# Kernel tuning notes

Hardware: AMD Instinct MI355X
Metric: run time of the kernel (lower is better)

Reference implementation:

```python
import jax, jax.numpy as jnp
import numpy as np

# ---- box encoding helpers ----

def _cv2_corners(b):
    # b: [..., 5] (cx, cy, w, h, angle) -> [..., 4, 2] rotated-rect vertices
    cx, cy, w, h, a = (b[..., i] for i in range(5))
    c, s = jnp.cos(a), jnp.sin(a)
    dx, dy = w * 0.5, h * 0.5
    lx = jnp.stack([-dx, dx, dx, -dx], axis=-1)   # [..., 4]
    ly = jnp.stack([-dy, -dy, dy, dy], axis=-1)
    x = cx[..., None] + lx * c[..., None] - ly * s[..., None]
    y = cy[..., None] + lx * s[..., None] + ly * c[..., None]
    return jnp.stack([x, y], axis=-1)


def _vertices_to_cv2(v):
    # v: [..., 4, 2] ordered vertices -> [..., 5] (cx, cy, w, h, angle)
    ctr = v.mean(axis=-2)
    e1 = v[..., 1, :] - v[..., 0, :]
    e2 = v[..., 3, :] - v[..., 0, :]
    w = jnp.linalg.norm(e1, axis=-1)
    h = jnp.linalg.norm(e2, axis=-1)
    ang = jnp.arctan2(e1[..., 1], e1[..., 0])
    return jnp.concatenate([ctr, w[..., None], h[..., None], ang[..., None]], axis=-1)


def _corners_to_hbb(corners):
    # [..., 4, 2] -> [..., 4] (x1, y1, x2, y2)
    return jnp.concatenate([corners.min(axis=-2), corners.max(axis=-2)], axis=-1)


def _box_iou(a, b):
    # a: [B, N, 4], b: [B, M, 4] -> [B, N, M] axis-aligned IoU
    lt = jnp.maximum(a[:, :, None, :2], b[:, None, :, :2])
    rb = jnp.minimum(a[:, :, None, 2:], b[:, None, :, 2:])
    wh = jnp.clip(rb - lt, 0.0)
    inter = wh[..., 0] * wh[..., 1]
    area_a = (a[..., 2] - a[..., 0]) * (a[..., 3] - a[..., 1])
    area_b = (b[..., 2] - b[..., 0]) * (b[..., 3] - b[..., 1])
    union = area_a[:, :, None] + area_b[:, None, :] - inter
    return inter / jnp.clip(union, 1e-7)


def setup_inputs() -> dict:
    key = jax.random.key(0)
    ks = jax.random.split(key, 6)
    B, N, M, C = 8, 16384, 128, 81

    def rand_boxes(k, shape):
        k1, k2, k3 = jax.random.split(k, 3)
        ctr = jax.random.uniform(k1, shape + (2,), minval=0.0, maxval=1000.0)
        wh = jax.random.uniform(k2, shape + (2,), minval=16.0, maxval=160.0)
        ang = jax.random.uniform(k3, shape + (1,), minval=-1.5, maxval=1.5)
        return jnp.concatenate([ctr, wh, ang], axis=-1)

    box_pred = rand_boxes(ks[0], (B, N))
    gt = rand_boxes(ks[1], (B, M))
    # seed the first M predictions near the GT so positives (IoU>=0.5) exist
    box_pred = box_pred.at[:, :M].set(gt + 2.0 * jax.random.normal(ks[2], gt.shape))
    regression_targets = _cv2_corners(gt)                     # [B, M, 4, 2] vertices
    classification_targets = jax.random.randint(ks[3], (B, M), 0, C - 1)
    class_pred = jax.random.normal(ks[4], (B, N, C))
    return {
        "box_pred": box_pred,
        "class_pred": class_pred,
        "regression_targets": regression_targets,
        "classification_targets": classification_targets,
        "n_samples": 256,
    }


def reference(box_pred, class_pred, regression_targets, classification_targets, n_samples):
    B = box_pred.shape[0]
    C = class_pred.shape[-1]
    background_cls = C - 1
    k_pos = n_samples // 2
    k_neg = n_samples - k_pos

    box_targets_cv2 = _vertices_to_cv2(regression_targets)           # [B, M, 5]
    hbb_pred = _corners_to_hbb(_cv2_corners(box_pred))               # [B, N, 4]
    hbb_tgt = _corners_to_hbb(regression_targets)                    # [B, M, 4]
    iou = _box_iou(hbb_pred, hbb_tgt)                                # [B, N, M]

    def per_image(iou_i, labels_i, logits_i, boxp_i, boxt_i):
        max_iou = iou_i.max(axis=-1)                                 # [N]
        match = iou_i.argmax(axis=-1)                                # [N] matched GT idx
        pos_mask = max_iou >= 0.5
        # sample up to k_pos positives (highest IoU) and k_neg negatives (lowest IoU)
        pos_score = jnp.where(pos_mask, max_iou, -1.0)
        _, pos_idx = jax.lax.top_k(pos_score, k_pos)
        pos_valid = pos_mask[pos_idx]
        neg_score = jnp.where(pos_mask, -jnp.inf, -max_iou)
        _, neg_idx = jax.lax.top_k(neg_score, k_neg)
        neg_valid = ~pos_mask[neg_idx]
        # classification targets: matched GT label for positives, background otherwise
        cls_target = jnp.where(pos_mask, labels_i[match], background_cls)
        sel_idx = jnp.concatenate([pos_idx, neg_idx])                # [n_samples]
        sel_valid = jnp.concatenate([pos_valid, neg_valid])
        logp = jax.nn.log_softmax(logits_i[sel_idx], axis=-1)        # [n_samples, C]
        nll = -jnp.take_along_axis(logp, cls_target[sel_idx][:, None], axis=1)[:, 0]
        cls_loss = jnp.sum(nll * sel_valid.astype(logp.dtype))
        rel_pred = boxp_i[pos_idx]                                   # [k_pos, 5]
        rel_gt = boxt_i[match[pos_idx]]                              # [k_pos, 5]
        d = jnp.abs(rel_pred - rel_gt)
        sl1 = jnp.where(d < 1.0, 0.5 * d * d, d - 0.5)
        regr_loss = jnp.sum(sl1 * pos_valid[:, None].astype(sl1.dtype))
        return cls_loss, regr_loss

    cls_l, reg_l = jax.vmap(per_image)(
        iou, classification_targets, class_pred, box_pred, box_targets_cv2
    )
    classification_loss = cls_l.sum() / B
    regression_loss = reg_l.sum() / B
    total_loss = classification_loss + regression_loss
    return total_loss, classification_loss, regression_loss
```

## Files before the change

kernel.cpp:

```cpp
#include <hip/hip_runtime.h>
#include <math.h>

#define B_ 8
#define N_ 16384
#define M_ 128
#define C_ 81

__global__ __launch_bounds__(256)
void iou_fused(const float* __restrict__ bp,
               const float* __restrict__ rt,
               float* __restrict__ miou,
               int* __restrict__ match,
               float* __restrict__ out) {
    __shared__ float sx1[M_], sy1[M_], sx2[M_], sy2[M_], sab[M_];
    int b = blockIdx.y;
    int n = blockIdx.x * blockDim.x + threadIdx.x;

    if (blockIdx.x == 0 && blockIdx.y == 0 && threadIdx.x < 3)
        out[threadIdx.x] = 0.0f;

    if (threadIdx.x < M_) {
        const float* v = rt + ((size_t)b * M_ + threadIdx.x) * 8;
        float x0 = v[0], y0 = v[1], x1 = v[2], y1 = v[3];
        float x2 = v[4], y2 = v[5], x3 = v[6], y3 = v[7];
        float mnx = fminf(fminf(x0, x1), fminf(x2, x3));
        float mny = fminf(fminf(y0, y1), fminf(y2, y3));
        float mxx = fmaxf(fmaxf(x0, x1), fmaxf(x2, x3));
        float mxy = fmaxf(fmaxf(y0, y1), fmaxf(y2, y3));
        sx1[threadIdx.x] = mnx; sy1[threadIdx.x] = mny;
        sx2[threadIdx.x] = mxx; sy2[threadIdx.x] = mxy;
        sab[threadIdx.x] = (mxx - mnx) * (mxy - mny);
    }
    __syncthreads();

    const float* p = bp + ((size_t)b * N_ + n) * 5;
    float cx = p[0], cy = p[1], w = p[2], h = p[3], a = p[4];
    float c = cosf(a), s = sinf(a);
    float dx = w * 0.5f, dy = h * 0.5f;
    float ex = fabsf(dx * c) + fabsf(dy * s);
    float ey = fabsf(dx * s) + fabsf(dy * c);
    float ax1 = cx - ex, ay1 = cy - ey, ax2 = cx + ex, ay2 = cy + ey;
    float area_a = (ax2 - ax1) * (ay2 - ay1);

    float bin = -1.0f, bun = 1.0f;
    int bm = 0;
#pragma unroll 4
    for (int m = 0; m < M_; m++) {
        float lx = fmaxf(ax1, sx1[m]), ly = fmaxf(ay1, sy1[m]);
        float rx = fminf(ax2, sx2[m]), ry = fminf(ay2, sy2[m]);
        float ww = fmaxf(rx - lx, 0.0f), hh = fmaxf(ry - ly, 0.0f);
        float inter = ww * hh;
        float uni = fmaxf(area_a + sab[m] - inter, 1e-7f);
        bool better = inter * bun > bin * uni;
        bin = better ? inter : bin;
        bun = better ? uni : bun;
        bm = better ? m : bm;
    }
    miou[(size_t)b * N_ + n] = bin / bun;
    match[(size_t)b * N_ + n] = bm;
}

__device__ __forceinline__ unsigned bredu(unsigned v, unsigned* slot) {
#pragma unroll
    for (int o = 32; o; o >>= 1) v += __shfl_down(v, o);
    if ((threadIdx.x & 63) == 0) slot[threadIdx.x >> 6] = v;
    __syncthreads();
    unsigned r = 0;
#pragma unroll
    for (int i = 0; i < 16; i++) r += slot[i];
    return r;
}

__device__ __forceinline__ float bredf(float v, float* slot) {
#pragma unroll
    for (int o = 32; o; o >>= 1) v += __shfl_down(v, o);
    if ((threadIdx.x & 63) == 0) slot[threadIdx.x >> 6] = v;
    __syncthreads();
    float r = 0.f;
#pragma unroll
    for (int i = 0; i < 16; i++) r += slot[i];
    return r;
}

__global__ __launch_bounds__(1024)
void select_loss(const float* __restrict__ miou, const int* __restrict__ match,
                 const float* __restrict__ logits, const float* __restrict__ bp,
                 const float* __restrict__ rt, const int* __restrict__ labels,
                 const int* __restrict__ ns_ptr, float* __restrict__ out) {
    int type = blockIdx.x;
    int b = blockIdx.y;
    __shared__ float s_cv2[5][M_];
    __shared__ unsigned red[32] __attribute__((aligned(16)));
    __shared__ float fred[32] __attribute__((aligned(16)));
    __shared__ unsigned sel[256];
    __shared__ unsigned selcnt;

    int tid = threadIdx.x;
    int lane = tid & 63, wv = tid >> 6;
    if (tid == 0) selcnt = 0;

    if (tid < M_) {
        const float* v = rt + ((size_t)b * M_ + tid) * 8;
        float x0 = v[0], y0 = v[1], x1 = v[2], y1 = v[3];
        float x2 = v[4], y2 = v[5], x3 = v[6], y3 = v[7];
        s_cv2[0][tid] = (x0 + x1 + x2 + x3) * 0.25f;
        s_cv2[1][tid] = (y0 + y1 + y2 + y3) * 0.25f;
        float e1x = x1 - x0, e1y = y1 - y0;
        float e2x = x3 - x0, e2y = y3 - y0;
        s_cv2[2][tid] = sqrtf(e1x * e1x + e1y * e1y);
        s_cv2[3][tid] = sqrtf(e2x * e2x + e2y * e2y);
        s_cv2[4][tid] = atan2f(e1y, e1x);
    }

    int ns = ns_ptr[0];
    unsigned ktar = (type == 0) ? (unsigned)(ns / 2) : (unsigned)(ns - ns / 2);
    if (ktar > 256u) ktar = 256u;

    const float4* mi4 = (const float4*)(miou + (size_t)b * N_);
    int base = tid * 16;
    unsigned key[16];
    unsigned vcnt = 0;
#pragma unroll
    for (int q = 0; q < 4; q++) {
        float4 v4 = mi4[tid * 4 + q];
        float io[4] = {v4.x, v4.y, v4.z, v4.w};
#pragma unroll
        for (int j = 0; j < 4; j++) {
            bool pos = (io[j] >= 0.5f);
            unsigned k;
            if (type == 0) {
                if (pos) { k = ~(__float_as_uint(io[j]) | 0x80000000u); vcnt++; }
                else k = 0xFFFFFFFFu;
            } else {
                if (!pos) { k = __float_as_uint(io[j]) | 0x80000000u; vcnt++; }
                else k = 0xFFFFFFFFu;
            }
            key[q * 4 + j] = k;
        }
    }
    __syncthreads();

    int pc = 0;
    unsigned V = bredu(vcnt, red + 16 * ((pc++) & 1));
    unsigned keff = (ktar < V) ? ktar : V;

    if (keff == V) {
#pragma unroll
        for (int j = 0; j < 16; j++) {
            if (key[j] != 0xFFFFFFFFu) {
                unsigned p = atomicAdd(&selcnt, 1u);
                sel[p] = (unsigned)(base + j);
            }
        }
    } else {
        unsigned lo = 0, hi = 0xFFFFFFFFu;
        while (lo < hi) {
            unsigned mid = lo + ((hi - lo) >> 1);
            unsigned c = 0;
#pragma unroll
            for (int j = 0; j < 16; j++) c += (key[j] <= mid) ? 1u : 0u;
            unsigned tot = bredu(c, red + 16 * ((pc++) & 1));
            if (tot >= keff) hi = mid; else lo = mid + 1;
        }
        unsigned Ckey = lo;

        unsigned cl = 0, ce = 0;
#pragma unroll
        for (int j = 0; j < 16; j++) {
            cl += (key[j] < Ckey) ? 1u : 0u;
            ce += (key[j] == Ckey) ? 1u : 0u;
        }
        unsigned m = bredu(cl, red + 16 * ((pc++) & 1));
        unsigned e = keff - m;

        unsigned sc = ce;
#pragma unroll
        for (int o = 1; o < 64; o <<= 1) {
            unsigned t = __shfl_up(sc, o);
            if (lane >= o) sc += t;
        }
        unsigned* slot = red + 16 * ((pc++) & 1);
        if (lane == 63) slot[wv] = sc;
        __syncthreads();
        unsigned off = 0;
        for (int i = 0; i < wv; i++) off += slot[i];
        unsigned rank = off + sc - ce;

#pragma unroll
        for (int j = 0; j < 16; j++) {
            unsigned k = key[j];
            bool s = false;
            if (k < Ckey) s = true;
            else if (k == Ckey) { s = (rank < e); rank++; }
            if (s) {
                unsigned p = atomicAdd(&selcnt, 1u);
                sel[p] = (unsigned)(base + j);
            }
        }
    }
    __syncthreads();
    unsigned total_sel = selcnt;

    float cls_sum = 0.f, reg_sum = 0.f;
    {
        int g = tid >> 2, q = tid & 3;
        if ((unsigned)g < total_sel) {
            unsigned i = sel[g];
            const float* row = logits + ((size_t)b * N_ + i) * C_;
            int c0 = q * 21;
            int c1 = (c0 + 21 < C_) ? c0 + 21 : C_;
            float mx = -INFINITY;
            for (int c = c0; c < c1; c++) mx = fmaxf(mx, row[c]);
            mx = fmaxf(mx, __shfl_xor(mx, 1));
            mx = fmaxf(mx, __shfl_xor(mx, 2));
            float se = 0.f;
            for (int c = c0; c < c1; c++) se += expf(row[c] - mx);
            se += __shfl_xor(se, 1);
            se += __shfl_xor(se, 2);
            if (q == 0) {
                float lse = mx + logf(se);
                if (type == 0) {
                    int g_gt = match[(size_t)b * N_ + i];
                    int tc = labels[b * M_ + g_gt];
                    cls_sum = lse - row[tc];
                    const float* pp = bp + ((size_t)b * N_ + i) * 5;
#pragma unroll
                    for (int d = 0; d < 5; d++) {
                        float ad = fabsf(pp[d] - s_cv2[d][g_gt]);
                        reg_sum += (ad < 1.f) ? 0.5f * ad * ad : ad - 0.5f;
                    }
                } else {
                    cls_sum = lse - row[C_ - 1];
                }
            }
        }
    }
    float cs = bredf(cls_sum, fred + 16 * 0);
    float rs = bredf(reg_sum, fred + 16 * 1);
    if (tid == 0) {
        const float invB = 1.0f / (float)B_;
        atomicAdd(&out[0], (cs + rs) * invB);
        atomicAdd(&out[1], cs * invB);
        atomicAdd(&out[2], rs * invB);
    }
}

extern "C" void kernel_launch(void* const* d_in, const int* in_sizes, int n_in,
                              void* d_out, int out_size, void* d_ws, size_t ws_size,
                              hipStream_t stream) {
    const float* box_pred = (const float*)d_in[0];
    const float* class_pred = (const float*)d_in[1];
    const float* reg_tgt = (const float*)d_in[2];
    const int* cls_tgt = (const int*)d_in[3];
    const int* n_samples = (const int*)d_in[4];

    float* ws = (float*)d_ws;
    float* miou = ws;
    int* match = (int*)(miou + (size_t)B_ * N_);
    float* out = (float*)d_out;

    iou_fused<<<dim3(N_ / 256, B_), 256, 0, stream>>>(box_pred, reg_tgt, miou, match, out);
    select_loss<<<dim3(2, B_), 1024, 0, stream>>>(miou, match, class_pred, box_pred,
                                                  reg_tgt, cls_tgt, n_samples, out);
}
```

Baseline: 135.6 us.

## Shrink select block, ballot-based reductions, early threshold exit, hoist GT boxes

The select kernel now runs 512 threads with 32 keys per thread and sums counts across each wave using ballot/popcount bit-slices instead of shuffle chains. Negatives get an early check: if enough keys sit at the minimum value, the binary search is skipped and its ~32 block-wide reductions are avoided. GT axis-aligned boxes are precomputed once in a separate kernel and read from global memory inside the IoU loop instead of shared memory. This adds one kernel launch. The IoU loop now relies on cached global loads rather than LDS broadcast reads.

```diff
diff --git a/kernel.cpp b/kernel.cpp
--- a/kernel.cpp
+++ b/kernel.cpp
@@ -5,34 +5,34 @@
 #define N_ 16384
 #define M_ 128
 #define C_ 81
+#define TPB 512
+#define KPT 32
+#define NWAVE (TPB / 64)
 
 __global__ __launch_bounds__(256)
-void iou_fused(const float* __restrict__ bp,
-               const float* __restrict__ rt,
-               float* __restrict__ miou,
-               int* __restrict__ match,
-               float* __restrict__ out) {
-    __shared__ float sx1[M_], sy1[M_], sx2[M_], sy2[M_], sab[M_];
+void prep_gt(const float* __restrict__ rt, float* __restrict__ hbb8,
+             float* __restrict__ out) {
+    int g = blockIdx.x * blockDim.x + threadIdx.x;
+    if (blockIdx.x == 0 && threadIdx.x < 3) out[threadIdx.x] = 0.0f;
+    if (g >= B_ * M_) return;
+    const float* v = rt + (size_t)g * 8;
+    float x0 = v[0], y0 = v[1], x1 = v[2], y1 = v[3];
+    float x2 = v[4], y2 = v[5], x3 = v[6], y3 = v[7];
+    float mnx = fminf(fminf(x0, x1), fminf(x2, x3));
+    float mny = fminf(fminf(y0, y1), fminf(y2, y3));
+    float mxx = fmaxf(fmaxf(x0, x1), fmaxf(x2, x3));
+    float mxy = fmaxf(fmaxf(y0, y1), fmaxf(y2, y3));
+    float* o = hbb8 + (size_t)g * 8;
+    o[0] = mnx; o[1] = mny; o[2] = mxx; o[3] = mxy;
+    o[4] = (mxx - mnx) * (mxy - mny);
+    o[5] = 0.f; o[6] = 0.f; o[7] = 0.f;
+}
+
+__global__ __launch_bounds__(256)
+void iou_kernel(const float* __restrict__ bp, const float* __restrict__ hbb8,
+                float* __restrict__ miou, int* __restrict__ match) {
     int b = blockIdx.y;
     int n = blockIdx.x * blockDim.x + threadIdx.x;
-
-    if (blockIdx.x == 0 && blockIdx.y == 0 && threadIdx.x < 3)
-        out[threadIdx.x] = 0.0f;
-
-    if (threadIdx.x < M_) {
-        const float* v = rt + ((size_t)b * M_ + threadIdx.x) * 8;
-        float x0 = v[0], y0 = v[1], x1 = v[2], y1 = v[3];
-        float x2 = v[4], y2 = v[5], x3 = v[6], y3 = v[7];
-        float mnx = fminf(fminf(x0, x1), fminf(x2, x3));
-        float mny = fminf(fminf(y0, y1), fminf(y2, y3));
-        float mxx = fmaxf(fmaxf(x0, x1), fmaxf(x2, x3));
-        float mxy = fmaxf(fmaxf(y0, y1), fmaxf(y2, y3));
-        sx1[threadIdx.x] = mnx; sy1[threadIdx.x] = mny;
-        sx2[threadIdx.x] = mxx; sy2[threadIdx.x] = mxy;
-        sab[threadIdx.x] = (mxx - mnx) * (mxy - mny);
-    }
-    __syncthreads();
-
     const float* p = bp + ((size_t)b * N_ + n) * 5;
     float cx = p[0], cy = p[1], w = p[2], h = p[3], a = p[4];
     float c = cosf(a), s = sinf(a);
@@ -42,15 +42,19 @@
     float ax1 = cx - ex, ay1 = cy - ey, ax2 = cx + ex, ay2 = cy + ey;
     float area_a = (ax2 - ax1) * (ay2 - ay1);
 
+    const float* gbase = hbb8 + (size_t)b * M_ * 8;
     float bin = -1.0f, bun = 1.0f;
     int bm = 0;
 #pragma unroll 4
     for (int m = 0; m < M_; m++) {
-        float lx = fmaxf(ax1, sx1[m]), ly = fmaxf(ay1, sy1[m]);
-        float rx = fminf(ax2, sx2[m]), ry = fminf(ay2, sy2[m]);
+        float bx1 = gbase[m * 8 + 0], by1 = gbase[m * 8 + 1];
+        float bx2 = gbase[m * 8 + 2], by2 = gbase[m * 8 + 3];
+        float ab  = gbase[m * 8 + 4];
+        float lx = fmaxf(ax1, bx1), ly = fmaxf(ay1, by1);
+        float rx = fminf(ax2, bx2), ry = fminf(ay2, by2);
         float ww = fmaxf(rx - lx, 0.0f), hh = fmaxf(ry - ly, 0.0f);
         float inter = ww * hh;
-        float uni = fmaxf(area_a + sab[m] - inter, 1e-7f);
+        float uni = fmaxf(area_a + ab - inter, 1e-7f);
         bool better = inter * bun > bin * uni;
         bin = better ? inter : bin;
         bun = better ? uni : bun;
@@ -60,29 +64,25 @@
     match[(size_t)b * N_ + n] = bm;
 }
 
-__device__ __forceinline__ unsigned bredu(unsigned v, unsigned* slot) {
-#pragma unroll
-    for (int o = 32; o; o >>= 1) v += __shfl_down(v, o);
-    if ((threadIdx.x & 63) == 0) slot[threadIdx.x >> 6] = v;
+__device__ __forceinline__ unsigned wave_sum6(unsigned c) {
+    unsigned s = 0;
+#pragma unroll
+    for (int bit = 0; bit < 6; bit++)
+        s += (unsigned)__popcll(__ballot((c >> bit) & 1u)) << bit;
+    return s;
+}
+
+__device__ __forceinline__ unsigned bsum(unsigned c, unsigned* slot) {
+    unsigned ws = wave_sum6(c);
+    if ((threadIdx.x & 63) == 0) slot[threadIdx.x >> 6] = ws;
     __syncthreads();
     unsigned r = 0;
 #pragma unroll
-    for (int i = 0; i < 16; i++) r += slot[i];
+    for (int i = 0; i < NWAVE; i++) r += slot[i];
     return r;
 }
 
-__device__ __forceinline__ float bredf(float v, float* slot) {
-#pragma unroll
-    for (int o = 32; o; o >>= 1) v += __shfl_down(v, o);
-    if ((threadIdx.x & 63) == 0) slot[threadIdx.x >> 6] = v;
-    __syncthreads();
-    float r = 0.f;
-#pragma unroll
-    for (int i = 0; i < 16; i++) r += slot[i];
-    return r;
-}
-
-__global__ __launch_bounds__(1024)
+__global__ __launch_bounds__(TPB)
 void select_loss(const float* __restrict__ miou, const int* __restrict__ match,
                  const float* __restrict__ logits, const float* __restrict__ bp,
                  const float* __restrict__ rt, const int* __restrict__ labels,
@@ -90,8 +90,8 @@
     int type = blockIdx.x;
     int b = blockIdx.y;
     __shared__ float s_cv2[5][M_];
-    __shared__ unsigned red[32] __attribute__((aligned(16)));
-    __shared__ float fred[32] __attribute__((aligned(16)));
+    __shared__ unsigned red[2 * NWAVE] __attribute__((aligned(16)));
+    __shared__ float fredc[NWAVE], fredr[NWAVE];
     __shared__ unsigned sel[256];
     __shared__ unsigned selcnt;
 
@@ -117,12 +117,12 @@
     if (ktar > 256u) ktar = 256u;
 
     const float4* mi4 = (const float4*)(miou + (size_t)b * N_);
-    int base = tid * 16;
-    unsigned key[16];
+    int base = tid * KPT;
+    unsigned key[KPT];
     unsigned vcnt = 0;
 #pragma unroll
-    for (int q = 0; q < 4; q++) {
-        float4 v4 = mi4[tid * 4 + q];
+    for (int q = 0; q < KPT / 4; q++) {
+        float4 v4 = mi4[tid * (KPT / 4) + q];
         float io[4] = {v4.x, v4.y, v4.z, v4.w};
 #pragma unroll
         for (int j = 0; j < 4; j++) {
@@ -141,36 +141,47 @@
     __syncthreads();
 
     int pc = 0;
-    unsigned V = bredu(vcnt, red + 16 * ((pc++) & 1));
+    unsigned V = bsum(vcnt, red + NWAVE * ((pc++) & 1));
     unsigned keff = (ktar < V) ? ktar : V;
 
     if (keff == V) {
 #pragma unroll
-        for (int j = 0; j < 16; j++) {
+        for (int j = 0; j < KPT; j++) {
             if (key[j] != 0xFFFFFFFFu) {
                 unsigned p = atomicAdd(&selcnt, 1u);
                 sel[p] = (unsigned)(base + j);
             }
         }
     } else {
-        unsigned lo = 0, hi = 0xFFFFFFFFu;
-        while (lo < hi) {
-            unsigned mid = lo + ((hi - lo) >> 1);
-            unsigned c = 0;
-#pragma unroll
-            for (int j = 0; j < 16; j++) c += (key[j] <= mid) ? 1u : 0u;
-            unsigned tot = bredu(c, red + 16 * ((pc++) & 1));
-            if (tot >= keff) hi = mid; else lo = mid + 1;
-        }
-        unsigned Ckey = lo;
+        unsigned Ckey;
+        bool found = false;
+        if (type == 1) {
+            unsigned cmin = 0;
+#pragma unroll
+            for (int j = 0; j < KPT; j++) cmin += (key[j] <= 0x80000000u) ? 1u : 0u;
+            unsigned tot = bsum(cmin, red + NWAVE * ((pc++) & 1));
+            if (tot >= keff) { Ckey = 0x80000000u; found = true; }
+        }
+        if (!found) {
+            unsigned lo = 0, hi = 0xFFFFFFFFu;
+            while (lo < hi) {
+                unsigned mid = lo + ((hi - lo) >> 1);
+                unsigned c = 0;
+#pragma unroll
+                for (int j = 0; j < KPT; j++) c += (key[j] <= mid) ? 1u : 0u;
+                unsigned tot = bsum(c, red + NWAVE * ((pc++) & 1));
+                if (tot >= keff) hi = mid; else lo = mid + 1;
+            }
+            Ckey = lo;
+        }
 
         unsigned cl = 0, ce = 0;
 #pragma unroll
-        for (int j = 0; j < 16; j++) {
+        for (int j = 0; j < KPT; j++) {
             cl += (key[j] < Ckey) ? 1u : 0u;
             ce += (key[j] == Ckey) ? 1u : 0u;
         }
-        unsigned m = bredu(cl, red + 16 * ((pc++) & 1));
+        unsigned m = bsum(cl, red + NWAVE * ((pc++) & 1));
         unsigned e = keff - m;
 
         unsigned sc = ce;
@@ -179,7 +190,7 @@
             unsigned t = __shfl_up(sc, o);
             if (lane >= o) sc += t;
         }
-        unsigned* slot = red + 16 * ((pc++) & 1);
+        unsigned* slot = red + NWAVE * ((pc++) & 1);
         if (lane == 63) slot[wv] = sc;
         __syncthreads();
         unsigned off = 0;
@@ -187,7 +198,7 @@
         unsigned rank = off + sc - ce;
 
 #pragma unroll
-        for (int j = 0; j < 16; j++) {
+        for (int j = 0; j < KPT; j++) {
             unsigned k = key[j];
             bool s = false;
             if (k < Ckey) s = true;
@@ -202,42 +213,49 @@
     unsigned total_sel = selcnt;
 
     float cls_sum = 0.f, reg_sum = 0.f;
-    {
-        int g = tid >> 2, q = tid & 3;
-        if ((unsigned)g < total_sel) {
-            unsigned i = sel[g];
-            const float* row = logits + ((size_t)b * N_ + i) * C_;
-            int c0 = q * 21;
-            int c1 = (c0 + 21 < C_) ? c0 + 21 : C_;
-            float mx = -INFINITY;
-            for (int c = c0; c < c1; c++) mx = fmaxf(mx, row[c]);
-            mx = fmaxf(mx, __shfl_xor(mx, 1));
-            mx = fmaxf(mx, __shfl_xor(mx, 2));
-            float se = 0.f;
-            for (int c = c0; c < c1; c++) se += expf(row[c] - mx);
-            se += __shfl_xor(se, 1);
-            se += __shfl_xor(se, 2);
-            if (q == 0) {
-                float lse = mx + logf(se);
-                if (type == 0) {
-                    int g_gt = match[(size_t)b * N_ + i];
-                    int tc = labels[b * M_ + g_gt];
-                    cls_sum = lse - row[tc];
-                    const float* pp = bp + ((size_t)b * N_ + i) * 5;
-#pragma unroll
-                    for (int d = 0; d < 5; d++) {
-                        float ad = fabsf(pp[d] - s_cv2[d][g_gt]);
-                        reg_sum += (ad < 1.f) ? 0.5f * ad * ad : ad - 0.5f;
-                    }
-                } else {
-                    cls_sum = lse - row[C_ - 1];
+    int q = tid & 3;
+    for (unsigned sm = (unsigned)(tid >> 2); sm < total_sel; sm += TPB / 4) {
+        unsigned i = sel[sm];
+        const float* row = logits + ((size_t)b * N_ + i) * C_;
+        int c0 = q * 21;
+        int c1 = (c0 + 21 < C_) ? c0 + 21 : C_;
+        float mx = -INFINITY;
+        for (int c = c0; c < c1; c++) mx = fmaxf(mx, row[c]);
+        mx = fmaxf(mx, __shfl_xor(mx, 1));
+        mx = fmaxf(mx, __shfl_xor(mx, 2));
+        float se = 0.f;
+        for (int c = c0; c < c1; c++) se += expf(row[c] - mx);
+        se += __shfl_xor(se, 1);
+        se += __shfl_xor(se, 2);
+        if (q == 0) {
+            float lse = mx + logf(se);
+            if (type == 0) {
+                int g_gt = match[(size_t)b * N_ + i];
+                int tc = labels[b * M_ + g_gt];
+                cls_sum += lse - row[tc];
+                const float* pp = bp + ((size_t)b * N_ + i) * 5;
+#pragma unroll
+                for (int d = 0; d < 5; d++) {
+                    float ad = fabsf(pp[d] - s_cv2[d][g_gt]);
+                    reg_sum += (ad < 1.f) ? 0.5f * ad * ad : ad - 0.5f;
                 }
-            }
-        }
-    }
-    float cs = bredf(cls_sum, fred + 16 * 0);
-    float rs = bredf(reg_sum, fred + 16 * 1);
+            } else {
+                cls_sum += lse - row[C_ - 1];
+            }
+        }
+    }
+
+#pragma unroll
+    for (int o = 32; o; o >>= 1) {
+        cls_sum += __shfl_down(cls_sum, o);
+        reg_sum += __shfl_down(reg_sum, o);
+    }
+    if (lane == 0) { fredc[wv] = cls_sum; fredr[wv] = reg_sum; }
+    __syncthreads();
     if (tid == 0) {
+        float cs = 0.f, rs = 0.f;
+#pragma unroll
+        for (int i = 0; i < NWAVE; i++) { cs += fredc[i]; rs += fredr[i]; }
         const float invB = 1.0f / (float)B_;
         atomicAdd(&out[0], (cs + rs) * invB);
         atomicAdd(&out[1], cs * invB);
@@ -255,11 +273,13 @@
     const int* n_samples = (const int*)d_in[4];
 
     float* ws = (float*)d_ws;
-    float* miou = ws;
+    float* hbb8 = ws;
+    float* miou = hbb8 + (size_t)B_ * M_ * 8;
     int* match = (int*)(miou + (size_t)B_ * N_);
     float* out = (float*)d_out;
 
-    iou_fused<<<dim3(N_ / 256, B_), 256, 0, stream>>>(box_pred, reg_tgt, miou, match, out);
-    select_loss<<<dim3(2, B_), 1024, 0, stream>>>(miou, match, class_pred, box_pred,
-                                                  reg_tgt, cls_tgt, n_samples, out);
-}
+    prep_gt<<<(B_ * M_ + 255) / 256, 256, 0, stream>>>(reg_tgt, hbb8, out);
+    iou_kernel<<<dim3(N_ / 256, B_), 256, 0, stream>>>(box_pred, hbb8, miou, match);
+    select_loss<<<dim3(2, B_), TPB, 0, stream>>>(miou, match, class_pred, box_pred,
+                                                 reg_tgt, cls_tgt, n_samples, out);
+}
```

Result: slower. 145.8 us (+7.6%).
